# Kernel tuning notes

Measured on AMD Instinct MI355X. Metric: run time of the kernel, lower is better.

## Reference

```python
import jax, jax.numpy as jnp
import numpy as np

N = 16384      # n_samples
D = 1024       # embedding_size
C = 16         # number of classes (balanced so every anchor has a positive)
MARGIN = 1.0
EPS = 1e-6


def setup_inputs() -> dict:
    rng = np.random.default_rng(0)
    labels = np.arange(N) % C
    rng.shuffle(labels)
    # positive index: same label, different sample (random within-class rotation)
    pos = np.empty(N, dtype=np.int64)
    for c in range(C):
        idx = np.nonzero(labels == c)[0]
        off = rng.integers(1, len(idx), size=len(idx))
        pos[idx] = idx[(np.arange(len(idx)) + off) % len(idx)]
    # negative index: any sample with a different label (rejection-resample on host)
    neg = rng.integers(0, N, size=N)
    while True:
        bad = labels[neg] == labels
        if not bad.any():
            break
        neg[bad] = rng.integers(0, N, size=int(bad.sum()))
    key = jax.random.key(0)
    embeddings = jax.random.normal(key, (N, D), dtype=jnp.float32)
    return {
        "embeddings": embeddings,
        "labels": jnp.asarray(labels, dtype=jnp.int64),
        "pos_idx": jnp.asarray(pos, dtype=jnp.int64),
        "neg_idx": jnp.asarray(neg, dtype=jnp.int64),
    }


def reference(embeddings, labels, pos_idx, neg_idx):
    # F.normalize(p=2, dim=1, eps=1e-6): x / max(||x||_2, eps)
    norm = jnp.sqrt(jnp.sum(embeddings * embeddings, axis=1, keepdims=True))
    e = embeddings / jnp.maximum(norm, EPS)                      # [N, D]

    def pdist(a, b):
        # F.pairwise_distance adds eps to the difference; module adds another +eps
        return jnp.sqrt(jnp.sum((a - b + EPS) ** 2, axis=1)) + EPS

    d_pos = pdist(e, e[pos_idx])                                 # [N]
    d_neg = pdist(e, e[neg_idx])                                 # [N]
    positive_loss = d_pos ** 2
    negative_loss = jnp.maximum(MARGIN - d_neg, EPS) ** 2
    total = jnp.sum(positive_loss) + jnp.sum(negative_loss)
    return total / (2.0 * N)
```

## Files before the change

kernel.cpp:

```cpp
#include <hip/hip_runtime.h>

#define NROWS 16384
#define DIM   1024
#define MARGIN_F 1.0f
#define EPS_F 1e-6f

__global__ __launch_bounds__(256) void row_loss_kernel(
    const float* __restrict__ emb,
    const int*   __restrict__ pos_idx,
    const int*   __restrict__ neg_idx,
    float*       __restrict__ losses)
{
    const int row  = blockIdx.x;
    const int tid  = threadIdx.x;
    const int lane = tid & 63;
    const int wid  = tid >> 6;

    const int p = pos_idx[row];
    const int n = neg_idx[row];

    const float4* xi = (const float4*)(emb + (size_t)row * DIM);
    const float4* xp = (const float4*)(emb + (size_t)p   * DIM);
    const float4* xn = (const float4*)(emb + (size_t)n   * DIM);

    const float4 a = xi[tid];
    const float4 b = xp[tid];
    const float4 c = xn[tid];

    float ni = a.x*a.x + a.y*a.y + a.z*a.z + a.w*a.w;
    float np_ = b.x*b.x + b.y*b.y + b.z*b.z + b.w*b.w;
    float nn = c.x*c.x + c.y*c.y + c.z*c.z + c.w*c.w;

    #pragma unroll
    for (int off = 32; off > 0; off >>= 1) {
        ni  += __shfl_down(ni,  off, 64);
        np_ += __shfl_down(np_, off, 64);
        nn  += __shfl_down(nn,  off, 64);
    }

    __shared__ float sm[3][4];
    __shared__ float scales[3];
    if (lane == 0) { sm[0][wid] = ni; sm[1][wid] = np_; sm[2][wid] = nn; }
    __syncthreads();
    if (tid == 0) {
        float si = sm[0][0] + sm[0][1] + sm[0][2] + sm[0][3];
        float sp = sm[1][0] + sm[1][1] + sm[1][2] + sm[1][3];
        float sn = sm[2][0] + sm[2][1] + sm[2][2] + sm[2][3];
        scales[0] = 1.0f / fmaxf(sqrtf(si), EPS_F);
        scales[1] = 1.0f / fmaxf(sqrtf(sp), EPS_F);
        scales[2] = 1.0f / fmaxf(sqrtf(sn), EPS_F);
    }
    __syncthreads();
    const float si = scales[0];
    const float sp = scales[1];
    const float sn = scales[2];

    float sum_p = 0.0f, sum_n = 0.0f;
    {
        float t;
        t = a.x*si - b.x*sp + EPS_F; sum_p += t*t;
        t = a.y*si - b.y*sp + EPS_F; sum_p += t*t;
        t = a.z*si - b.z*sp + EPS_F; sum_p += t*t;
        t = a.w*si - b.w*sp + EPS_F; sum_p += t*t;
        t = a.x*si - c.x*sn + EPS_F; sum_n += t*t;
        t = a.y*si - c.y*sn + EPS_F; sum_n += t*t;
        t = a.z*si - c.z*sn + EPS_F; sum_n += t*t;
        t = a.w*si - c.w*sn + EPS_F; sum_n += t*t;
    }

    #pragma unroll
    for (int off = 32; off > 0; off >>= 1) {
        sum_p += __shfl_down(sum_p, off, 64);
        sum_n += __shfl_down(sum_n, off, 64);
    }
    if (lane == 0) { sm[0][wid] = sum_p; sm[1][wid] = sum_n; }
    __syncthreads();
    if (tid == 0) {
        float s_pos = sm[0][0] + sm[0][1] + sm[0][2] + sm[0][3];
        float s_neg = sm[1][0] + sm[1][1] + sm[1][2] + sm[1][3];
        float d_pos = sqrtf(s_pos) + EPS_F;
        float d_neg = sqrtf(s_neg) + EPS_F;
        float pl = d_pos * d_pos;
        float mq = fmaxf(MARGIN_F - d_neg, EPS_F);
        float nl = mq * mq;
        losses[row] = pl + nl;
    }
}

__global__ __launch_bounds__(256) void final_reduce_kernel(
    const float* __restrict__ losses,
    float*       __restrict__ out)
{
    const int tid  = threadIdx.x;
    const int lane = tid & 63;
    const int wid  = tid >> 6;

    float s = 0.0f;
    for (int i = tid; i < NROWS; i += 256) s += losses[i];

    #pragma unroll
    for (int off = 32; off > 0; off >>= 1) s += __shfl_down(s, off, 64);

    __shared__ float sm[4];
    if (lane == 0) sm[wid] = s;
    __syncthreads();
    if (tid == 0) {
        float total = sm[0] + sm[1] + sm[2] + sm[3];
        out[0] = total / (2.0f * (float)NROWS);
    }
}

extern "C" void kernel_launch(void* const* d_in, const int* in_sizes, int n_in,
                              void* d_out, int out_size, void* d_ws, size_t ws_size,
                              hipStream_t stream) {
    const float* emb = (const float*)d_in[0];
    const int* pos = (const int*)d_in[2];
    const int* neg = (const int*)d_in[3];

    float* losses = (float*)d_ws;
    float* out    = (float*)d_out;

    row_loss_kernel<<<NROWS, 256, 0, stream>>>(emb, pos, neg, losses);
    final_reduce_kernel<<<1, 256, 0, stream>>>(losses, out);
}
```

Before: 127.2 us.

## Map one wavefront per row to remove block barriers and shared-memory reductions

The row kernel now assigns one 64-lane wavefront per row, four rows per 256-thread block. Each lane holds four float4 values per input row, and norms and distances are reduced entirely with xor shuffles. This removes three __syncthreads barriers and the shared-memory round trips per row, and cuts the block count fourfold. The final reduce uses 1024 threads with float4 loads. The trade-off is more registers per lane and fewer loads in flight per wavefront.

```diff
diff --git a/kernel.cpp b/kernel.cpp
--- a/kernel.cpp
+++ b/kernel.cpp
@@ -2,6 +2,8 @@
 
 #define NROWS 16384
 #define DIM   1024
+#define F4_PER_ROW 256
+#define F4_PER_LANE 4
 #define MARGIN_F 1.0f
 #define EPS_F 1e-6f
 
@@ -11,10 +13,10 @@
     const int*   __restrict__ neg_idx,
     float*       __restrict__ losses)
 {
-    const int row  = blockIdx.x;
     const int tid  = threadIdx.x;
     const int lane = tid & 63;
     const int wid  = tid >> 6;
+    const int row  = blockIdx.x * 4 + wid;
 
     const int p = pos_idx[row];
     const int n = neg_idx[row];
@@ -23,71 +25,62 @@
     const float4* xp = (const float4*)(emb + (size_t)p   * DIM);
     const float4* xn = (const float4*)(emb + (size_t)n   * DIM);
 
-    const float4 a = xi[tid];
-    const float4 b = xp[tid];
-    const float4 c = xn[tid];
-
-    float ni = a.x*a.x + a.y*a.y + a.z*a.z + a.w*a.w;
-    float np_ = b.x*b.x + b.y*b.y + b.z*b.z + b.w*b.w;
-    float nn = c.x*c.x + c.y*c.y + c.z*c.z + c.w*c.w;
-
+    float4 a[F4_PER_LANE], b[F4_PER_LANE], c[F4_PER_LANE];
     #pragma unroll
-    for (int off = 32; off > 0; off >>= 1) {
-        ni  += __shfl_down(ni,  off, 64);
-        np_ += __shfl_down(np_, off, 64);
-        nn  += __shfl_down(nn,  off, 64);
+    for (int j = 0; j < F4_PER_LANE; ++j) {
+        a[j] = xi[lane + 64 * j];
+        b[j] = xp[lane + 64 * j];
+        c[j] = xn[lane + 64 * j];
     }
 
-    __shared__ float sm[3][4];
-    __shared__ float scales[3];
-    if (lane == 0) { sm[0][wid] = ni; sm[1][wid] = np_; sm[2][wid] = nn; }
-    __syncthreads();
-    if (tid == 0) {
-        float si = sm[0][0] + sm[0][1] + sm[0][2] + sm[0][3];
-        float sp = sm[1][0] + sm[1][1] + sm[1][2] + sm[1][3];
-        float sn = sm[2][0] + sm[2][1] + sm[2][2] + sm[2][3];
-        scales[0] = 1.0f / fmaxf(sqrtf(si), EPS_F);
-        scales[1] = 1.0f / fmaxf(sqrtf(sp), EPS_F);
-        scales[2] = 1.0f / fmaxf(sqrtf(sn), EPS_F);
+    float ni = 0.f, np_ = 0.f, nn = 0.f;
+    #pragma unroll
+    for (int j = 0; j < F4_PER_LANE; ++j) {
+        ni  = fmaf(a[j].x, a[j].x, ni);  ni  = fmaf(a[j].y, a[j].y, ni);
+        ni  = fmaf(a[j].z, a[j].z, ni);  ni  = fmaf(a[j].w, a[j].w, ni);
+        np_ = fmaf(b[j].x, b[j].x, np_); np_ = fmaf(b[j].y, b[j].y, np_);
+        np_ = fmaf(b[j].z, b[j].z, np_); np_ = fmaf(b[j].w, b[j].w, np_);
+        nn  = fmaf(c[j].x, c[j].x, nn);  nn  = fmaf(c[j].y, c[j].y, nn);
+        nn  = fmaf(c[j].z, c[j].z, nn);  nn  = fmaf(c[j].w, c[j].w, nn);
     }
-    __syncthreads();
-    const float si = scales[0];
-    const float sp = scales[1];
-    const float sn = scales[2];
+    #pragma unroll
+    for (int m = 1; m < 64; m <<= 1) {
+        ni  += __shfl_xor(ni,  m, 64);
+        np_ += __shfl_xor(np_, m, 64);
+        nn  += __shfl_xor(nn,  m, 64);
+    }
+    const float si = 1.0f / fmaxf(sqrtf(ni),  EPS_F);
+    const float sp = 1.0f / fmaxf(sqrtf(np_), EPS_F);
+    const float sn = 1.0f / fmaxf(sqrtf(nn),  EPS_F);
 
-    float sum_p = 0.0f, sum_n = 0.0f;
-    {
+    float sum_p = 0.f, sum_n = 0.f;
+    #pragma unroll
+    for (int j = 0; j < F4_PER_LANE; ++j) {
         float t;
-        t = a.x*si - b.x*sp + EPS_F; sum_p += t*t;
-        t = a.y*si - b.y*sp + EPS_F; sum_p += t*t;
-        t = a.z*si - b.z*sp + EPS_F; sum_p += t*t;
-        t = a.w*si - b.w*sp + EPS_F; sum_p += t*t;
-        t = a.x*si - c.x*sn + EPS_F; sum_n += t*t;
-        t = a.y*si - c.y*sn + EPS_F; sum_n += t*t;
-        t = a.z*si - c.z*sn + EPS_F; sum_n += t*t;
-        t = a.w*si - c.w*sn + EPS_F; sum_n += t*t;
+        t = fmaf(a[j].x, si, -b[j].x * sp) + EPS_F; sum_p = fmaf(t, t, sum_p);
+        t = fmaf(a[j].y, si, -b[j].y * sp) + EPS_F; sum_p = fmaf(t, t, sum_p);
+        t = fmaf(a[j].z, si, -b[j].z * sp) + EPS_F; sum_p = fmaf(t, t, sum_p);
+        t = fmaf(a[j].w, si, -b[j].w * sp) + EPS_F; sum_p = fmaf(t, t, sum_p);
+        t = fmaf(a[j].x, si, -c[j].x * sn) + EPS_F; sum_n = fmaf(t, t, sum_n);
+        t = fmaf(a[j].y, si, -c[j].y * sn) + EPS_F; sum_n = fmaf(t, t, sum_n);
+        t = fmaf(a[j].z, si, -c[j].z * sn) + EPS_F; sum_n = fmaf(t, t, sum_n);
+        t = fmaf(a[j].w, si, -c[j].w * sn) + EPS_F; sum_n = fmaf(t, t, sum_n);
+    }
+    #pragma unroll
+    for (int m = 1; m < 64; m <<= 1) {
+        sum_p += __shfl_xor(sum_p, m, 64);
+        sum_n += __shfl_xor(sum_n, m, 64);
     }
 
-    #pragma unroll
-    for (int off = 32; off > 0; off >>= 1) {
-        sum_p += __shfl_down(sum_p, off, 64);
-        sum_n += __shfl_down(sum_n, off, 64);
-    }
-    if (lane == 0) { sm[0][wid] = sum_p; sm[1][wid] = sum_n; }
-    __syncthreads();
-    if (tid == 0) {
-        float s_pos = sm[0][0] + sm[0][1] + sm[0][2] + sm[0][3];
-        float s_neg = sm[1][0] + sm[1][1] + sm[1][2] + sm[1][3];
-        float d_pos = sqrtf(s_pos) + EPS_F;
-        float d_neg = sqrtf(s_neg) + EPS_F;
-        float pl = d_pos * d_pos;
+    if (lane == 0) {
+        float d_pos = sqrtf(sum_p) + EPS_F;
+        float d_neg = sqrtf(sum_n) + EPS_F;
         float mq = fmaxf(MARGIN_F - d_neg, EPS_F);
-        float nl = mq * mq;
-        losses[row] = pl + nl;
+        losses[row] = d_pos * d_pos + mq * mq;
     }
 }
 
-__global__ __launch_bounds__(256) void final_reduce_kernel(
+__global__ __launch_bounds__(1024) void final_reduce_kernel(
     const float* __restrict__ losses,
     float*       __restrict__ out)
 {
@@ -95,17 +88,23 @@
     const int lane = tid & 63;
     const int wid  = tid >> 6;
 
+    const float4* l4 = (const float4*)losses;
     float s = 0.0f;
-    for (int i = tid; i < NROWS; i += 256) s += losses[i];
+    #pragma unroll
+    for (int j = 0; j < 4; ++j) {
+        float4 v = l4[tid + 1024 * j];
+        s += v.x + v.y + v.z + v.w;
+    }
+    #pragma unroll
+    for (int m = 1; m < 64; m <<= 1) s += __shfl_xor(s, m, 64);
 
-    #pragma unroll
-    for (int off = 32; off > 0; off >>= 1) s += __shfl_down(s, off, 64);
-
-    __shared__ float sm[4];
+    __shared__ float sm[16];
     if (lane == 0) sm[wid] = s;
     __syncthreads();
     if (tid == 0) {
-        float total = sm[0] + sm[1] + sm[2] + sm[3];
+        float total = 0.f;
+        #pragma unroll
+        for (int w = 0; w < 16; ++w) total += sm[w];
         out[0] = total / (2.0f * (float)NROWS);
     }
 }
@@ -120,6 +119,6 @@
     float* losses = (float*)d_ws;
     float* out    = (float*)d_out;
 
-    row_loss_kernel<<<NROWS, 256, 0, stream>>>(emb, pos, neg, losses);
-    final_reduce_kernel<<<1, 256, 0, stream>>>(losses, out);
+    row_loss_kernel<<<NROWS / 4, 256, 0, stream>>>(emb, pos, neg, losses);
+    final_reduce_kernel<<<1, 1024, 0, stream>>>(losses, out);
 }
```

Measured after the change: 110.8 us. 12.9% less time.
